# Kernel optimization log

Hardware: AMD Instinct MI355X
Metric: run time of the kernel (lower is better)

## Reference

```python
import jax, jax.numpy as jnp
import numpy as np

D_MODEL = 1024
N_HEADS = 16
D_HEAD = D_MODEL // N_HEADS
HIDDEN = 4 * D_MODEL
EPS = 1e-5


def setup_inputs() -> dict:
    key = jax.random.key(0)
    ks = jax.random.split(key, 8)
    B, C = 4, 2048
    s = lambda fan_in: 1.0 / np.sqrt(fan_in)
    return {
        "x": jax.random.normal(ks[0], (B, C, D_MODEL), jnp.float32),
        "gamma1": jnp.ones((D_MODEL,), jnp.float32),
        "beta1": jnp.zeros((D_MODEL,), jnp.float32),
        "W_qkv": jax.random.normal(ks[1], (D_MODEL, 3 * D_MODEL), jnp.float32) * s(D_MODEL),
        "b_qkv": jnp.zeros((3 * D_MODEL,), jnp.float32),
        "W_o": jax.random.normal(ks[2], (D_MODEL, D_MODEL), jnp.float32) * s(D_MODEL),
        "b_o": jnp.zeros((D_MODEL,), jnp.float32),
        "gamma2": jnp.ones((D_MODEL,), jnp.float32),
        "beta2": jnp.zeros((D_MODEL,), jnp.float32),
        "W1": jax.random.normal(ks[3], (D_MODEL, HIDDEN), jnp.float32) * s(D_MODEL),
        "b1": jnp.zeros((HIDDEN,), jnp.float32),
        "W2": jax.random.normal(ks[4], (HIDDEN, D_MODEL), jnp.float32) * s(HIDDEN),
        "b2": jnp.zeros((D_MODEL,), jnp.float32),
    }


def _layernorm(x, gamma, beta):
    mean = jnp.mean(x, axis=-1, keepdims=True)
    var = jnp.mean(jnp.square(x - mean), axis=-1, keepdims=True)
    return gamma * (x - mean) / jnp.sqrt(var + EPS) + beta


def _attention(x, W_qkv, b_qkv, W_o, b_o):
    B, C, D = x.shape
    qkv = x @ W_qkv + b_qkv                                  # (B,C,3D)
    qkv = qkv.reshape(B, C, 3, N_HEADS, D_HEAD)
    qkv = jnp.transpose(qkv, (2, 0, 3, 1, 4))                # (3,B,H,C,dh)
    Q, K, V = qkv[0], qkv[1], qkv[2]
    scores = jnp.einsum("bhqd,bhkd->bhqk", Q, K) / np.sqrt(D_HEAD)
    causal = jnp.tril(jnp.ones((C, C), bool))
    scores = jnp.where(causal, scores, -jnp.inf)
    weights = jax.nn.softmax(scores, axis=-1)
    out = jnp.einsum("bhqk,bhkd->bhqd", weights, V)          # (B,H,C,dh)
    out = jnp.transpose(out, (0, 2, 1, 3)).reshape(B, C, D)
    return out @ W_o + b_o


def reference(x, gamma1, beta1, W_qkv, b_qkv, W_o, b_o, gamma2, beta2, W1, b1, W2, b2):
    x = x + _attention(_layernorm(x, gamma1, beta1), W_qkv, b_qkv, W_o, b_o)
    h = _layernorm(x, gamma2, beta2)
    h = jax.nn.gelu(h @ W1 + b1, approximate=False) @ W2 + b2
    return x + h
```

## Files before the change

### kernel.cpp

```cpp
#include <hip/hip_runtime.h>
#include <hip/hip_bf16.h>
#include <math.h>


typedef __attribute__((ext_vector_type(8))) short short8;
typedef __attribute__((ext_vector_type(4))) float f32x4;

typedef const __attribute__((address_space(1))) unsigned int glb_u32;
typedef __attribute__((address_space(3))) unsigned int lds_u32;

__device__ __forceinline__ void gload16(const void* g, void* l) {
  __builtin_amdgcn_global_load_lds((glb_u32*)g, (lds_u32*)l, 16, 0, 0);
}

__device__ __forceinline__ unsigned short f2bf(float f) {
  union { __hip_bfloat16 h; unsigned short u; } c;
  c.h = __float2bfloat16(f);
  return c.u;
}

__device__ __forceinline__ float bf2f(unsigned short u) {
  union { unsigned int u; float f; } c;
  c.u = ((unsigned int)u) << 16;
  return c.f;
}

__device__ __forceinline__ float gelu_exact(float v) {
  return 0.5f * v * (1.0f + erff(v * 0.7071067811865475f));
}

__global__ __launch_bounds__(256) void transpose_convert(
    const float* __restrict__ in, unsigned short* __restrict__ outp, int K, int N) {
  __shared__ float tile[32][33];
  const int bk = blockIdx.x * 32, bn = blockIdx.y * 32;
  const int t = threadIdx.x;
  const int r = t >> 5, c = t & 31;
#pragma unroll
  for (int p = 0; p < 4; ++p)
    tile[r + p * 8][c] = in[(size_t)(bk + r + p * 8) * N + bn + c];
  __syncthreads();
#pragma unroll
  for (int p = 0; p < 4; ++p)
    outp[(size_t)(bn + r + p * 8) * K + bk + c] = f2bf(tile[c][r + p * 8]);
}

__global__ __launch_bounds__(256) void transpose_v(
    const unsigned short* __restrict__ qkv, unsigned short* __restrict__ vT) {
  __shared__ unsigned short tile[64][68];
  const int bh = blockIdx.y;
  const int b = bh >> 4, h = bh & 15;
  const int q0 = blockIdx.x * 64;
  const int t = threadIdx.x;
  const int r = t >> 3, c8 = t & 7;
#pragma unroll
  for (int p = 0; p < 2; ++p) {
    const int q = r + p * 32;
    short8 v = *(const short8*)(qkv + (size_t)(b * 2048 + q0 + q) * 3072 + 2048 + h * 64 + c8 * 8);
    *(short8*)(&tile[q][c8 * 8]) = v;
  }
  __syncthreads();
#pragma unroll
  for (int p = 0; p < 2; ++p) {
    const int d = r + p * 32;
    short8 v;
#pragma unroll
    for (int j = 0; j < 8; ++j) v[j] = tile[c8 * 8 + j][d];
    *(short8*)(vT + ((size_t)bh * 64 + d) * 2048 + q0 + c8 * 8) = v;
  }
}

__global__ __launch_bounds__(256) void layernorm_k(
    const float* __restrict__ x, const float* __restrict__ gamma,
    const float* __restrict__ beta, unsigned short* __restrict__ out) {
  const int row = blockIdx.x;
  const int t = threadIdx.x;
  const float4 v = ((const float4*)(x + (size_t)row * 1024))[t];
  float s = v.x + v.y + v.z + v.w;
  float sq = v.x * v.x + v.y * v.y + v.z * v.z + v.w * v.w;
#pragma unroll
  for (int sh = 32; sh >= 1; sh >>= 1) {
    s += __shfl_xor(s, sh);
    sq += __shfl_xor(sq, sh);
  }
  __shared__ float ps[4], pq[4];
  if ((t & 63) == 0) { ps[t >> 6] = s; pq[t >> 6] = sq; }
  __syncthreads();
  s = ps[0] + ps[1] + ps[2] + ps[3];
  sq = pq[0] + pq[1] + pq[2] + pq[3];
  const float mean = s * (1.0f / 1024.0f);
  const float var = sq * (1.0f / 1024.0f) - mean * mean;
  const float rstd = rsqrtf(var + 1e-5f);
  const float4 g = ((const float4*)gamma)[t];
  const float4 be = ((const float4*)beta)[t];
  ushort4 ov;
  ov.x = f2bf(g.x * (v.x - mean) * rstd + be.x);
  ov.y = f2bf(g.y * (v.y - mean) * rstd + be.y);
  ov.z = f2bf(g.z * (v.z - mean) * rstd + be.z);
  ov.w = f2bf(g.w * (v.w - mean) * rstd + be.w);
  ((ushort4*)(out + (size_t)row * 1024))[t] = ov;
}

template <int EPI>
__global__ __launch_bounds__(256) void gemm_bt(
    const unsigned short* __restrict__ A, const unsigned short* __restrict__ Bt,
    const float* __restrict__ bias, const float* __restrict__ res,
    void* __restrict__ outp, int M, int N, int K) {
  __shared__ unsigned short lA[128 * 64];
  __shared__ unsigned short lB[128 * 64];
  const int t = threadIdx.x;
  const int lane = t & 63;
  const int wave = t >> 6;
  const int l15 = lane & 15, l4 = lane >> 4;

  const int gx = gridDim.x;
  int lin = blockIdx.y * gx + blockIdx.x;
  const int cpx = (gx * gridDim.y) >> 3;
  lin = (lin & 7) * cpx + (lin >> 3);
  const int m0 = (lin / gx) * 128, n0 = (lin % gx) * 128;
  const int wm = (wave >> 1) * 64, wn = (wave & 1) * 64;

  f32x4 acc[4][4];
#pragma unroll
  for (int a_ = 0; a_ < 4; ++a_)
#pragma unroll
    for (int b_ = 0; b_ < 4; ++b_) acc[a_][b_] = f32x4{0.f, 0.f, 0.f, 0.f};

  const int s_sub = lane >> 3;
  const int s_c8 = lane & 7;

  for (int k0 = 0; k0 < K; k0 += 64) {
    __syncthreads();
#pragma unroll
    for (int j = 0; j < 4; ++j) {
      const int chunk = wave * 4 + j;
      const int r = chunk * 8 + s_sub;
      const int c8s = s_c8 ^ (r & 7);
      gload16(A + (size_t)(m0 + r) * K + k0 + c8s * 8, lA + chunk * 512);
      gload16(Bt + (size_t)(n0 + r) * K + k0 + c8s * 8, lB + chunk * 512);
    }
    __syncthreads();
#pragma unroll
    for (int ks = 0; ks < 2; ++ks) {
      short8 af[4], bf[4];
#pragma unroll
      for (int mf = 0; mf < 4; ++mf) {
        const int r = wm + mf * 16 + l15;
        af[mf] = *(const short8*)(lA + r * 64 + (((ks * 4 + l4) ^ (r & 7)) * 8));
      }
#pragma unroll
      for (int nf = 0; nf < 4; ++nf) {
        const int r = wn + nf * 16 + l15;
        bf[nf] = *(const short8*)(lB + r * 64 + (((ks * 4 + l4) ^ (r & 7)) * 8));
      }
#pragma unroll
      for (int mf = 0; mf < 4; ++mf)
#pragma unroll
        for (int nf = 0; nf < 4; ++nf)
          acc[mf][nf] = __builtin_amdgcn_mfma_f32_16x16x32_bf16(
              af[mf], bf[nf], acc[mf][nf], 0, 0, 0);
    }
  }
#pragma unroll
  for (int mf = 0; mf < 4; ++mf)
#pragma unroll
    for (int i = 0; i < 4; ++i) {
      const int gm = m0 + wm + mf * 16 + l4 * 4 + i;
#pragma unroll
      for (int nf = 0; nf < 4; ++nf) {
        const int gn = n0 + wn + nf * 16 + l15;
        float v = acc[mf][nf][i] + bias[gn];
        if constexpr (EPI == 1) v = gelu_exact(v);
        if constexpr (EPI == 2) {
          v += res[(size_t)gm * N + gn];
          ((float*)outp)[(size_t)gm * N + gn] = v;
        } else {
          ((unsigned short*)outp)[(size_t)gm * N + gn] = f2bf(v);
        }
      }
    }
}

template <bool MASK>
__device__ __forceinline__ void attn_tile(
    int kt, int q0, const short8 (&qf)[2][2], f32x4 (&o)[2][4], f32x4 (&os)[2],
    float (&mrow)[2][4],
    const unsigned short* lK, const unsigned short* lV,
    unsigned short* lp, int l15, int l4) {
  f32x4 s[2][4];
#pragma unroll
  for (int mf = 0; mf < 2; ++mf)
#pragma unroll
    for (int nf = 0; nf < 4; ++nf) s[mf][nf] = f32x4{0.f, 0.f, 0.f, 0.f};
#pragma unroll
  for (int ks = 0; ks < 2; ++ks) {
    short8 kf[4];
#pragma unroll
    for (int nf = 0; nf < 4; ++nf) {
      const int r = nf * 16 + l15;
      kf[nf] = *(const short8*)(lK + r * 64 + (((ks * 4 + l4) ^ (r & 7)) * 8));
    }
#pragma unroll
    for (int mf = 0; mf < 2; ++mf)
#pragma unroll
      for (int nf = 0; nf < 4; ++nf)
        s[mf][nf] = __builtin_amdgcn_mfma_f32_16x16x32_bf16(
            qf[mf][ks], kf[nf], s[mf][nf], 0, 0, 0);
  }
  if constexpr (MASK) {
#pragma unroll
    for (int mf = 0; mf < 2; ++mf)
#pragma unroll
      for (int i = 0; i < 4; ++i) {
        const int gq = q0 + mf * 16 + l4 * 4 + i;
#pragma unroll
        for (int nf = 0; nf < 4; ++nf) {
          const int gk = kt * 64 + nf * 16 + l15;
          s[mf][nf][i] = (gk <= gq) ? s[mf][nf][i] : -1e30f;
        }
      }
  }
  float alpha[2][4];
#pragma unroll
  for (int mf = 0; mf < 2; ++mf)
#pragma unroll
    for (int i = 0; i < 4; ++i) {
      float mx = fmaxf(fmaxf(s[mf][0][i], s[mf][1][i]),
                       fmaxf(s[mf][2][i], s[mf][3][i]));
#pragma unroll
      for (int sh = 1; sh < 16; sh <<= 1) mx = fmaxf(mx, __shfl_xor(mx, sh));
      const float mnew = fmaxf(mrow[mf][i], mx);
      alpha[mf][i] = __expf(mrow[mf][i] - mnew);
      mrow[mf][i] = mnew;
#pragma unroll
      for (int nf = 0; nf < 4; ++nf)
        s[mf][nf][i] = __expf(s[mf][nf][i] - mnew);
    }
#pragma unroll
  for (int mf = 0; mf < 2; ++mf) {
#pragma unroll
    for (int nf = 0; nf < 4; ++nf)
#pragma unroll
      for (int i = 0; i < 4; ++i) o[mf][nf][i] *= alpha[mf][i];
#pragma unroll
    for (int i = 0; i < 4; ++i) os[mf][i] *= alpha[mf][i];
  }
#pragma unroll
  for (int mf = 0; mf < 2; ++mf)
#pragma unroll
    for (int nf = 0; nf < 4; ++nf)
#pragma unroll
      for (int i = 0; i < 4; ++i) {
        const int qr = mf * 16 + l4 * 4 + i;
        const int kb = (nf * 16 + l15) * 2;
        const int byt = qr * 128 + (kb ^ ((qr & 7) << 4));
        lp[byt >> 1] = f2bf(s[mf][nf][i]);
      }
  const short8 ones = {16256, 16256, 16256, 16256, 16256, 16256, 16256, 16256};
#pragma unroll
  for (int ks = 0; ks < 2; ++ks) {
    short8 pf[2], vf[4];
#pragma unroll
    for (int mf = 0; mf < 2; ++mf) {
      const int r = mf * 16 + l15;
      pf[mf] = *(const short8*)(lp + r * 64 + (((ks * 4 + l4) ^ (r & 7)) * 8));
    }
#pragma unroll
    for (int nf = 0; nf < 4; ++nf) {
      const int r = nf * 16 + l15;
      vf[nf] = *(const short8*)(lV + r * 64 + (((ks * 4 + l4) ^ (r & 7)) * 8));
    }
#pragma unroll
    for (int mf = 0; mf < 2; ++mf) {
      os[mf] = __builtin_amdgcn_mfma_f32_16x16x32_bf16(pf[mf], ones, os[mf], 0, 0, 0);
#pragma unroll
      for (int nf = 0; nf < 4; ++nf)
        o[mf][nf] = __builtin_amdgcn_mfma_f32_16x16x32_bf16(
            pf[mf], vf[nf], o[mf][nf], 0, 0, 0);
    }
  }
}

__global__ __launch_bounds__(256, 2) void attn_kernel(
    const unsigned short* __restrict__ qkv, const unsigned short* __restrict__ vT,
    unsigned short* __restrict__ attno) {
  __shared__ unsigned short lK[64 * 64];
  __shared__ unsigned short lV[64 * 64];
  __shared__ unsigned short lP[4][32 * 64];

  const int bh = blockIdx.x;
  const int qb = 15 - blockIdx.y;
  const int b = bh >> 4, h = bh & 15;
  const int t = threadIdx.x;
  const int wave = t >> 6, lane = t & 63;
  const int l15 = lane & 15, l4 = lane >> 4;

  const unsigned short* qkvb = qkv + (size_t)b * 2048 * 3072;
  const unsigned short* vTb = vT + (size_t)bh * 64 * 2048;
  const int q0 = qb * 128 + wave * 32;

  short8 qf[2][2];
#pragma unroll
  for (int mf = 0; mf < 2; ++mf)
#pragma unroll
    for (int ks = 0; ks < 2; ++ks) {
      const int qr = q0 + mf * 16 + l15;
      const int d = ks * 32 + l4 * 8;
      short8 raw = *(const short8*)(qkvb + (size_t)qr * 3072 + h * 64 + d);
#pragma unroll
      for (int j = 0; j < 8; ++j)
        qf[mf][ks][j] = (short)f2bf(bf2f((unsigned short)raw[j]) * 0.125f);
    }

  f32x4 o[2][4], os[2];
  float mrow[2][4];
#pragma unroll
  for (int mf = 0; mf < 2; ++mf) {
    os[mf] = f32x4{0.f, 0.f, 0.f, 0.f};
#pragma unroll
    for (int i = 0; i < 4; ++i) mrow[mf][i] = -1e30f;
#pragma unroll
    for (int nf = 0; nf < 4; ++nf) o[mf][nf] = f32x4{0.f, 0.f, 0.f, 0.f};
  }

  const int s_sub = lane >> 3, s_c8 = lane & 7;
  const int ktiles = qb * 2 + 2;
  for (int kt = 0; kt < ktiles; ++kt) {
    __syncthreads();
#pragma unroll
    for (int j = 0; j < 2; ++j) {
      const int chunk = wave * 2 + j;
      const int r = chunk * 8 + s_sub;
      const int c8s = s_c8 ^ (r & 7);
      gload16(qkvb + (size_t)(kt * 64 + r) * 3072 + 1024 + h * 64 + c8s * 8,
              lK + chunk * 512);
      gload16(vTb + (size_t)r * 2048 + kt * 64 + c8s * 8, lV + chunk * 512);
    }
    __syncthreads();

    if ((kt * 64) <= (q0 + 31)) {
      if ((kt * 64 + 63) <= q0)
        attn_tile<false>(kt, q0, qf, o, os, mrow, lK, lV, lP[wave], l15, l4);
      else
        attn_tile<true>(kt, q0, qf, o, os, mrow, lK, lV, lP[wave], l15, l4);
    }
  }

#pragma unroll
  for (int mf = 0; mf < 2; ++mf)
#pragma unroll
    for (int i = 0; i < 4; ++i) {
      const float inv = 1.0f / os[mf][i];
      const int gq = q0 + mf * 16 + l4 * 4 + i;
#pragma unroll
      for (int nf = 0; nf < 4; ++nf) {
        const int gd = nf * 16 + l15;
        attno[(size_t)(b * 2048 + gq) * 1024 + h * 64 + gd] =
            f2bf(o[mf][nf][i] * inv);
      }
    }
}

extern "C" void kernel_launch(void* const* d_in, const int* in_sizes, int n_in,
                              void* d_out, int out_size, void* d_ws, size_t ws_size,
                              hipStream_t stream) {
  const float* x    = (const float*)d_in[0];
  const float* g1   = (const float*)d_in[1];
  const float* be1  = (const float*)d_in[2];
  const float* Wqkv = (const float*)d_in[3];
  const float* bqkv = (const float*)d_in[4];
  const float* Wo   = (const float*)d_in[5];
  const float* bo   = (const float*)d_in[6];
  const float* g2   = (const float*)d_in[7];
  const float* be2  = (const float*)d_in[8];
  const float* W1   = (const float*)d_in[9];
  const float* b1   = (const float*)d_in[10];
  const float* W2   = (const float*)d_in[11];
  const float* b2   = (const float*)d_in[12];
  float* out = (float*)d_out;
  char* ws = (char*)d_ws;

  const size_t MB = 1024ull * 1024ull;
  unsigned short* qkv_g    = (unsigned short*)(ws + 0);
  unsigned short* ln1_attn = (unsigned short*)(ws + 64 * MB);
  float*          x2       = (float*)(ws + 80 * MB);
  unsigned short* vT       = (unsigned short*)(ws + 80 * MB);
  unsigned short* hbuf     = (unsigned short*)(ws + 112 * MB);
  unsigned short* wqkv_bt  = (unsigned short*)(ws + 128 * MB);
  unsigned short* wo_bt    = (unsigned short*)(ws + 134 * MB);
  unsigned short* w1_bt    = (unsigned short*)(ws + 136 * MB);
  unsigned short* w2_bt    = (unsigned short*)(ws + 144 * MB);

  transpose_convert<<<dim3(1024 / 32, 3072 / 32), 256, 0, stream>>>(Wqkv, wqkv_bt, 1024, 3072);
  transpose_convert<<<dim3(1024 / 32, 1024 / 32), 256, 0, stream>>>(Wo, wo_bt, 1024, 1024);
  transpose_convert<<<dim3(1024 / 32, 4096 / 32), 256, 0, stream>>>(W1, w1_bt, 1024, 4096);
  transpose_convert<<<dim3(4096 / 32, 1024 / 32), 256, 0, stream>>>(W2, w2_bt, 4096, 1024);

  layernorm_k<<<8192, 256, 0, stream>>>(x, g1, be1, ln1_attn);

  gemm_bt<0><<<dim3(3072 / 128, 8192 / 128), 256, 0, stream>>>(
      ln1_attn, wqkv_bt, bqkv, nullptr, qkv_g, 8192, 3072, 1024);

  transpose_v<<<dim3(2048 / 64, 64), 256, 0, stream>>>(qkv_g, vT);

  attn_kernel<<<dim3(64, 16), 256, 0, stream>>>(qkv_g, vT, ln1_attn);

  gemm_bt<2><<<dim3(1024 / 128, 8192 / 128), 256, 0, stream>>>(
      ln1_attn, wo_bt, bo, x, x2, 8192, 1024, 1024);

  layernorm_k<<<8192, 256, 0, stream>>>(x2, g2, be2, hbuf);

  gemm_bt<1><<<dim3(4096 / 128, 8192 / 128), 256, 0, stream>>>(
      hbuf, w1_bt, b1, nullptr, qkv_g, 8192, 4096, 1024);

  gemm_bt<2><<<dim3(1024 / 128, 8192 / 128), 256, 0, stream>>>(
      qkv_g, w2_bt, b2, x2, out, 8192, 1024, 4096);
}
```

Before: 524.0 us.

## Replace GEMM with 4-slot LDS ring pipeline and larger tiles for wide GEMMs

Replaces the synchronous load-then-compute GEMM with a templated kernel that keeps a four-slot LDS ring of K=32 stages. It prefetches three stages ahead using async global-to-LDS loads, explicit vmcnt waits and raw barriers, and raises wave priority around the MFMA block. The QKV and W1 GEMMs move to 256x256 tiles with 8 waves, while the output-projection and W2 GEMMs keep 128x128 tiles. The goal is to hide global load latency behind matrix math and to improve operand reuse on the large GEMMs. In exchange it uses more LDS and registers per block, and it relies on hand-coded waitcnt values being correct.

```diff
diff --git a/kernel.cpp b/kernel.cpp
--- a/kernel.cpp
+++ b/kernel.cpp
@@ -100,75 +100,116 @@
   ((ushort4*)(out + (size_t)row * 1024))[t] = ov;
 }
 
-template <int EPI>
-__global__ __launch_bounds__(256) void gemm_bt(
+template <int BM, int BN, int WM, int WN, int EPI>
+__global__ __launch_bounds__(WM * WN * 64, 2) void gemm_ring(
     const unsigned short* __restrict__ A, const unsigned short* __restrict__ Bt,
     const float* __restrict__ bias, const float* __restrict__ res,
     void* __restrict__ outp, int M, int N, int K) {
-  __shared__ unsigned short lA[128 * 64];
-  __shared__ unsigned short lB[128 * 64];
+  constexpr int NW = WM * WN;
+  constexpr int PWM = BM / WM, PWN = BN / WN;
+  constexpr int FM = PWM / 16, FN = PWN / 16;
+  constexpr int ACH = BM / 16;
+  constexpr int SLOT = (BM + BN) * 32;
+
+  __shared__ unsigned short lds[4 * SLOT];
+
   const int t = threadIdx.x;
-  const int lane = t & 63;
-  const int wave = t >> 6;
+  const int lane = t & 63, wave = t >> 6;
   const int l15 = lane & 15, l4 = lane >> 4;
+  const int wm = wave / WN, wn = wave % WN;
 
   const int gx = gridDim.x;
   int lin = blockIdx.y * gx + blockIdx.x;
   const int cpx = (gx * gridDim.y) >> 3;
   lin = (lin & 7) * cpx + (lin >> 3);
-  const int m0 = (lin / gx) * 128, n0 = (lin % gx) * 128;
-  const int wm = (wave >> 1) * 64, wn = (wave & 1) * 64;
-
-  f32x4 acc[4][4];
-#pragma unroll
-  for (int a_ = 0; a_ < 4; ++a_)
-#pragma unroll
-    for (int b_ = 0; b_ < 4; ++b_) acc[a_][b_] = f32x4{0.f, 0.f, 0.f, 0.f};
-
-  const int s_sub = lane >> 3;
-  const int s_c8 = lane & 7;
-
-  for (int k0 = 0; k0 < K; k0 += 64) {
-    __syncthreads();
+  const int m0 = (lin / gx) * BM, n0 = (lin % gx) * BN;
+
+  const int lr = lane >> 2, lc = lane & 3;
+
+  f32x4 acc[FM][FN];
+#pragma unroll
+  for (int f = 0; f < FM; ++f)
+#pragma unroll
+    for (int n = 0; n < FN; ++n) acc[f][n] = f32x4{0.f, 0.f, 0.f, 0.f};
+
+  const int nt = K >> 5;
+
+  auto STAGE = [&](int slot, int kt) {
+    const int k0 = kt * 32;
+    unsigned short* sb = lds + slot * SLOT;
 #pragma unroll
     for (int j = 0; j < 4; ++j) {
-      const int chunk = wave * 4 + j;
-      const int r = chunk * 8 + s_sub;
-      const int c8s = s_c8 ^ (r & 7);
-      gload16(A + (size_t)(m0 + r) * K + k0 + c8s * 8, lA + chunk * 512);
-      gload16(Bt + (size_t)(n0 + r) * K + k0 + c8s * 8, lB + chunk * 512);
-    }
-    __syncthreads();
-#pragma unroll
-    for (int ks = 0; ks < 2; ++ks) {
-      short8 af[4], bf[4];
-#pragma unroll
-      for (int mf = 0; mf < 4; ++mf) {
-        const int r = wm + mf * 16 + l15;
-        af[mf] = *(const short8*)(lA + r * 64 + (((ks * 4 + l4) ^ (r & 7)) * 8));
+      const int c = wave + NW * j;
+      if (c < ACH) {
+        const int r = c * 16 + lr;
+        const int kc = lc ^ ((r >> 1) & 3);
+        gload16(A + (size_t)(m0 + r) * K + k0 + kc * 8, sb + c * 512);
+      } else {
+        const int r = (c - ACH) * 16 + lr;
+        const int kc = lc ^ ((r >> 1) & 3);
+        gload16(Bt + (size_t)(n0 + r) * K + k0 + kc * 8,
+                sb + BM * 32 + (c - ACH) * 512);
       }
-#pragma unroll
-      for (int nf = 0; nf < 4; ++nf) {
-        const int r = wn + nf * 16 + l15;
-        bf[nf] = *(const short8*)(lB + r * 64 + (((ks * 4 + l4) ^ (r & 7)) * 8));
-      }
-#pragma unroll
-      for (int mf = 0; mf < 4; ++mf)
-#pragma unroll
-        for (int nf = 0; nf < 4; ++nf)
-          acc[mf][nf] = __builtin_amdgcn_mfma_f32_16x16x32_bf16(
-              af[mf], bf[nf], acc[mf][nf], 0, 0, 0);
-    }
-  }
-#pragma unroll
-  for (int mf = 0; mf < 4; ++mf)
+    }
+  };
+
+  auto COMPUTE = [&](int slot) {
+    const unsigned short* sa = lds + slot * SLOT;
+    const unsigned short* sbb = sa + BM * 32;
+    short8 af[FM], bf[FN];
+#pragma unroll
+    for (int f = 0; f < FM; ++f) {
+      const int r = wm * PWM + f * 16 + l15;
+      af[f] = *(const short8*)(sa + r * 32 + ((l4 ^ ((r >> 1) & 3)) << 3));
+    }
+#pragma unroll
+    for (int n = 0; n < FN; ++n) {
+      const int r = wn * PWN + n * 16 + l15;
+      bf[n] = *(const short8*)(sbb + r * 32 + ((l4 ^ ((r >> 1) & 3)) << 3));
+    }
+    __builtin_amdgcn_s_setprio(1);
+#pragma unroll
+    for (int f = 0; f < FM; ++f)
+#pragma unroll
+      for (int n = 0; n < FN; ++n)
+        acc[f][n] = __builtin_amdgcn_mfma_f32_16x16x32_bf16(
+            af[f], bf[n], acc[f][n], 0, 0, 0);
+    __builtin_amdgcn_s_setprio(0);
+  };
+
+  STAGE(0, 0); STAGE(1, 1); STAGE(2, 2);
+  int kt = 0;
+  for (; kt < nt - 3; ++kt) {
+    STAGE((kt + 3) & 3, kt + 3);
+    __builtin_amdgcn_sched_barrier(0);
+    __builtin_amdgcn_s_waitcnt(0xF7C);
+    __builtin_amdgcn_s_barrier();
+    COMPUTE(kt & 3);
+    __builtin_amdgcn_s_barrier();
+  }
+  __builtin_amdgcn_s_waitcnt(0xF78);
+  __builtin_amdgcn_s_barrier();
+  COMPUTE(kt & 3);
+  __builtin_amdgcn_s_barrier();
+  ++kt;
+  __builtin_amdgcn_s_waitcnt(0xF74);
+  __builtin_amdgcn_s_barrier();
+  COMPUTE(kt & 3);
+  __builtin_amdgcn_s_barrier();
+  ++kt;
+  __builtin_amdgcn_s_waitcnt(0xF70);
+  __builtin_amdgcn_s_barrier();
+  COMPUTE(kt & 3);
+
+#pragma unroll
+  for (int f = 0; f < FM; ++f)
 #pragma unroll
     for (int i = 0; i < 4; ++i) {
-      const int gm = m0 + wm + mf * 16 + l4 * 4 + i;
-#pragma unroll
-      for (int nf = 0; nf < 4; ++nf) {
-        const int gn = n0 + wn + nf * 16 + l15;
-        float v = acc[mf][nf][i] + bias[gn];
+      const int gm = m0 + wm * PWM + f * 16 + l4 * 4 + i;
+#pragma unroll
+      for (int n = 0; n < FN; ++n) {
+        const int gn = n0 + wn * PWN + n * 16 + l15;
+        float v = acc[f][n][i] + bias[gn];
         if constexpr (EPI == 1) v = gelu_exact(v);
         if constexpr (EPI == 2) {
           v += res[(size_t)gm * N + gn];
@@ -397,21 +438,21 @@
 
   layernorm_k<<<8192, 256, 0, stream>>>(x, g1, be1, ln1_attn);
 
-  gemm_bt<0><<<dim3(3072 / 128, 8192 / 128), 256, 0, stream>>>(
+  gemm_ring<256, 256, 2, 4, 0><<<dim3(3072 / 256, 8192 / 256), 512, 0, stream>>>(
       ln1_attn, wqkv_bt, bqkv, nullptr, qkv_g, 8192, 3072, 1024);
 
   transpose_v<<<dim3(2048 / 64, 64), 256, 0, stream>>>(qkv_g, vT);
 
   attn_kernel<<<dim3(64, 16), 256, 0, stream>>>(qkv_g, vT, ln1_attn);
 
-  gemm_bt<2><<<dim3(1024 / 128, 8192 / 128), 256, 0, stream>>>(
+  gemm_ring<128, 128, 2, 2, 2><<<dim3(1024 / 128, 8192 / 128), 256, 0, stream>>>(
       ln1_attn, wo_bt, bo, x, x2, 8192, 1024, 1024);
 
   layernorm_k<<<8192, 256, 0, stream>>>(x2, g2, be2, hbuf);
 
-  gemm_bt<1><<<dim3(4096 / 128, 8192 / 128), 256, 0, stream>>>(
+  gemm_ring<256, 256, 2, 4, 1><<<dim3(4096 / 256, 8192 / 256), 512, 0, stream>>>(
       hbuf, w1_bt, b1, nullptr, qkv_g, 8192, 4096, 1024);
 
-  gemm_bt<2><<<dim3(1024 / 128, 8192 / 128), 256, 0, stream>>>(
+  gemm_ring<128, 128, 2, 2, 2><<<dim3(1024 / 128, 8192 / 128), 256, 0, stream>>>(
       qkv_g, w2_bt, b2, x2, out, 8192, 1024, 4096);
 }
```

After: 534.3 us. About the same (+2.0%).
